# Optimization experiments

Hardware: AMD Instinct MI355X
Metric: run time of the kernel (lower is better)

Reference implementation:

```python
import jax, jax.numpy as jnp
import numpy as np

T, D, DFF, E, K = 2048, 1024, 2816, 8, 2


def setup_inputs() -> dict:
    key = jax.random.key(0)
    k1, k2, k3, k4, k5, k6 = jax.random.split(key, 6)
    return {
        "x": jax.random.normal(k1, (T, D), dtype=jnp.float32),
        "topk_weight": jax.random.uniform(k2, (T, K), dtype=jnp.float32),
        "gate_w": jax.random.normal(k3, (E, DFF, D), dtype=jnp.float32) * 0.02,
        "up_w": jax.random.normal(k4, (E, DFF, D), dtype=jnp.float32) * 0.02,
        "down_w": jax.random.normal(k5, (E, D, DFF), dtype=jnp.float32) * 0.02,
        "topk_ids": jax.random.randint(k6, (T, K), 0, E, dtype=jnp.int64),
    }


def reference(x, topk_weight, gate_w, up_w, down_w, topk_ids):
    # x: [T, D]; topk_ids/topk_weight: [T, K]
    # Per expert: SwiGLU MLP over all tokens, combined with the per-token
    # routing weight for that expert (0 if the expert was not selected).
    out = jnp.zeros_like(x)
    num_experts = gate_w.shape[0]
    for e in range(num_experts):
        h = jax.nn.silu(x @ gate_w[e].T) * (x @ up_w[e].T)  # [T, DFF]
        y = h @ down_w[e].T                                  # [T, D]
        # sum over top-k slots of routing weight where this expert was chosen
        w_e = jnp.sum(jnp.where(topk_ids == e, topk_weight, 0.0), axis=1)  # [T]
        out = out + y * w_e[:, None]
    return out
```

## Files before the change

kernel.cpp:

```cpp
#include <hip/hip_runtime.h>
#include <stdint.h>

typedef __attribute__((ext_vector_type(8))) __bf16 bf16x8;
typedef __attribute__((ext_vector_type(4))) float f32x4;
typedef __attribute__((ext_vector_type(8))) unsigned short ushort8;

#define T_TOK 2048
#define D_DIM 1024
#define DFF   2816
#define NEXP  8
#define NROWS 4096
#define BK    32
#define NW_ELEM (NEXP * DFF * D_DIM)
#define MAXTM2 24

#define SWZ(r,g) ((g) ^ (((r) >> 1) & 3))

#define TL_N    0
#define TL_BASE 16
#define TL_VAL  80
#define TL_EXP  144

__device__ __forceinline__ void lds_cp16(const void* g, void* l) {
  __builtin_amdgcn_global_load_lds(
      (const __attribute__((address_space(1))) void*)g,
      (__attribute__((address_space(3))) void*)l, 16, 0, 0);
}

__device__ __forceinline__ ushort8 pack_bf16x8(float4 a, float4 b) {
  union { __bf16 h[8]; ushort8 u; } r;
  r.h[0] = (__bf16)a.x; r.h[1] = (__bf16)a.y; r.h[2] = (__bf16)a.z; r.h[3] = (__bf16)a.w;
  r.h[4] = (__bf16)b.x; r.h[5] = (__bf16)b.y; r.h[6] = (__bf16)b.z; r.h[7] = (__bf16)b.w;
  return r.u;
}

__device__ __forceinline__ unsigned short f2bf(float f) {
  union { __bf16 h; unsigned short u; } r;
  r.h = (__bf16)f;
  return r.u;
}

__global__ __launch_bounds__(512) void routing_kernel(
    const int* __restrict__ ids, const float* __restrict__ w,
    int* __restrict__ cnt, int* __restrict__ off,
    int* __restrict__ tok, float* __restrict__ wgt, int* __restrict__ rowmap,
    int* __restrict__ tl2)
{
  __shared__ int s_cnt[NEXP];
  __shared__ int s_off[NEXP];
  const int lane = threadIdx.x & 63;
  const int e    = threadIdx.x >> 6;

  int total = 0;
  for (int c = 0; c < NROWS / 64; ++c) {
    int id = ids[c * 64 + lane];
    unsigned long long b = __ballot(id == e);
    total += __popcll(b);
  }
  if (lane == 0) s_cnt[e] = total;
  __syncthreads();
  if (threadIdx.x == 0) {
    int acc = 0, n2 = 0;
    for (int i = 0; i < NEXP; ++i) {
      s_off[i] = acc; off[i] = acc; cnt[i] = s_cnt[i];
      for (int j = 0; j < s_cnt[i]; j += 256) {
        tl2[TL_BASE + n2] = acc + j;
        tl2[TL_VAL  + n2] = min(256, s_cnt[i] - j);
        tl2[TL_EXP  + n2] = i;
        ++n2;
      }
      acc += s_cnt[i];
    }
    tl2[TL_N] = n2;
  }
  __syncthreads();
  int base = s_off[e];
  for (int c = 0; c < NROWS / 64; ++c) {
    int idx = c * 64 + lane;
    int id = ids[idx];
    bool m = (id == e);
    unsigned long long b = __ballot(m);
    int pos = __popcll(b & ((1ull << lane) - 1ull));
    if (m) {
      tok[base + pos] = idx >> 1;
      wgt[base + pos] = w[idx];
      rowmap[idx] = base + pos;
    }
    base += __popcll(b);
  }
}

__global__ __launch_bounds__(256) void gather_x_kernel(
    const float* __restrict__ x, const int* __restrict__ tok,
    unsigned short* __restrict__ xg)
{
  const int i = blockIdx.x;
  const int t = tok[i];
  const float4 v = ((const float4*)(x + (size_t)t * D_DIM))[threadIdx.x];
  ushort4 o;
  o.x = f2bf(v.x); o.y = f2bf(v.y); o.z = f2bf(v.z); o.w = f2bf(v.w);
  ((ushort4*)(xg + (size_t)i * D_DIM))[threadIdx.x] = o;
}

__global__ __launch_bounds__(256) void wconv_gu_kernel(
    const float* __restrict__ gw, const float* __restrict__ uw,
    unsigned short* __restrict__ gb, unsigned short* __restrict__ ub)
{
  const size_t n = NW_ELEM / 8;
  const size_t stride = (size_t)gridDim.x * blockDim.x;
  for (size_t i = (size_t)blockIdx.x * blockDim.x + threadIdx.x;
       i < 2 * n; i += stride) {
    const bool up = (i >= n);
    const size_t idx = (up ? i - n : i) * 8;
    const float* src = up ? uw : gw;
    unsigned short* dst = up ? ub : gb;
    float4 a = *(const float4*)(src + idx);
    float4 b = *(const float4*)(src + idx + 4);
    *(ushort8*)(dst + idx) = pack_bf16x8(a, b);
  }
}

#define BM_A 256
#define BN_A 64
#define NT_A (DFF / BN_A)
#define NWORK_A (MAXTM2 * NT_A)
#define WCD_BLKS 1024
#define NWG_A (NWORK_A + WCD_BLKS)
#define KT_A (D_DIM / BK)

__global__ __launch_bounds__(512) void moe_gateup_bf(
    const unsigned short* __restrict__ gbuf, const unsigned short* __restrict__ ubuf,
    const unsigned short* __restrict__ xg, const float* __restrict__ wgt,
    const int* __restrict__ tl2,
    unsigned short* __restrict__ hbuf,
    const float* __restrict__ down_w, unsigned short* __restrict__ dbuf)
{
  const int bid = blockIdx.x;
  const int ntm = tl2[TL_N];
  const int nwork = ntm * NT_A;
  const int tid = threadIdx.x;
  if (bid >= nwork) {
    if (bid >= NWORK_A) {
      const int c = bid - NWORK_A;
      const size_t stride = (size_t)WCD_BLKS * 512;
      for (size_t i = (size_t)c * 512 + tid; i < NW_ELEM / 8; i += stride) {
        const size_t idx = i * 8;
        float4 a = *(const float4*)(down_w + idx);
        float4 b = *(const float4*)(down_w + idx + 4);
        *(ushort8*)(dbuf + idx) = pack_bf16x8(a, b);
      }
    }
    return;
  }
  const int tile = bid % ntm;
  const int nt   = bid / ntm;
  const int row_base = tl2[TL_BASE + tile];
  const int valid    = tl2[TL_VAL  + tile];
  const int e        = tl2[TL_EXP  + tile];
  const int n0 = nt * BN_A;

  __shared__ __align__(16) unsigned short Alds[2][BM_A * BK];
  __shared__ __align__(16) unsigned short Bg[2][BN_A * BK];
  __shared__ __align__(16) unsigned short Bu[2][BN_A * BK];

  const int lane = tid & 63;
  const int wid = tid >> 6;
  const int wm = wid >> 1, wn = wid & 1;
  const int lhi = lane >> 4, llo = lane & 15;

  f32x4 accg[4][2], accu[4][2];
  #pragma unroll
  for (int i = 0; i < 4; ++i)
    #pragma unroll
    for (int j = 0; j < 2; ++j) {
      accg[i][j] = (f32x4){0.f, 0.f, 0.f, 0.f};
      accu[i][j] = (f32x4){0.f, 0.f, 0.f, 0.f};
    }

  const unsigned short* gb = gbuf + ((size_t)e * DFF + n0) * D_DIM;
  const unsigned short* ub = ubuf + ((size_t)e * DFF + n0) * D_DIM;

  const int ar0 = tid >> 2, ag = tid & 3;
  const int ar1 = ar0 + 128;
  const size_t a_src0 = (size_t)(row_base + min(ar0, valid - 1)) * D_DIM + SWZ(ar0, ag) * 8;
  const size_t a_src1 = (size_t)(row_base + min(ar1, valid - 1)) * D_DIM + SWZ(ar1, ag) * 8;
  const int q = tid & 255;
  const int br = q >> 2, bg2 = q & 3;
  const size_t b_src = (size_t)br * D_DIM + SWZ(br, bg2) * 8;
  const unsigned short* bsrc_base = (tid < 256) ? gb : ub;
  unsigned short* bdst0 = (tid < 256) ? &Bg[0][q * 8] : &Bu[0][q * 8];
  unsigned short* bdst1 = (tid < 256) ? &Bg[1][q * 8] : &Bu[1][q * 8];

  lds_cp16(xg + a_src0, &Alds[0][tid * 8]);
  lds_cp16(xg + a_src1, &Alds[0][(tid + 512) * 8]);
  lds_cp16(bsrc_base + b_src, bdst0);
  __syncthreads();

  for (int t = 0; t < KT_A; ++t) {
    const int cur = t & 1;
    const int kn = (t + 1 < KT_A) ? (t + 1) * BK : 0;

    lds_cp16(xg + a_src0 + kn, &Alds[cur ^ 1][tid * 8]);
    lds_cp16(xg + a_src1 + kn, &Alds[cur ^ 1][(tid + 512) * 8]);
    lds_cp16(bsrc_base + b_src + kn, cur ? bdst0 : bdst1);

    bf16x8 a[4], bgf[2], buf_[2];
    #pragma unroll
    for (int mi = 0; mi < 4; ++mi) {
      int row = wm * 64 + mi * 16 + llo;
      a[mi] = *(const bf16x8*)&Alds[cur][row * BK + SWZ(row, lhi) * 8];
    }
    #pragma unroll
    for (int ni = 0; ni < 2; ++ni) {
      int row = wn * 32 + ni * 16 + llo;
      bgf[ni]  = *(const bf16x8*)&Bg[cur][row * BK + SWZ(row, lhi) * 8];
      buf_[ni] = *(const bf16x8*)&Bu[cur][row * BK + SWZ(row, lhi) * 8];
    }
    #pragma unroll
    for (int mi = 0; mi < 4; ++mi)
      #pragma unroll
      for (int ni = 0; ni < 2; ++ni) {
        accg[mi][ni] = __builtin_amdgcn_mfma_f32_16x16x32_bf16(a[mi], bgf[ni], accg[mi][ni], 0, 0, 0);
        accu[mi][ni] = __builtin_amdgcn_mfma_f32_16x16x32_bf16(a[mi], buf_[ni], accu[mi][ni], 0, 0, 0);
      }
    __syncthreads();
  }

  #pragma unroll
  for (int mi = 0; mi < 4; ++mi) {
    #pragma unroll
    for (int r = 0; r < 4; ++r) {
      int row = wm * 64 + mi * 16 + lhi * 4 + r;
      if (row < valid) {
        int grow = row_base + row;
        float wv = wgt[grow];
        size_t base = (size_t)grow * DFF + n0 + wn * 32;
        #pragma unroll
        for (int ni = 0; ni < 2; ++ni) {
          float g = accg[mi][ni][r];
          float u = accu[mi][ni][r];
          float h = (g / (1.f + __expf(-g))) * u * wv;
          hbuf[base + ni * 16 + llo] = f2bf(h);
        }
      }
    }
  }
}

#define BM_B 256
#define BN_B 128
#define NT_B (D_DIM / BN_B)
#define SLICES_B 4
#define NWG_B (MAXTM2 * NT_B * SLICES_B)

template <bool USE_YBUF>
__global__ __launch_bounds__(512) void moe_down_bf(
    const unsigned short* __restrict__ dbuf,
    const unsigned short* __restrict__ hbuf,
    const int* __restrict__ tok,
    const int* __restrict__ tl2,
    float* __restrict__ ybuf_or_out)
{
  constexpr int KS = DFF / SLICES_B;
  constexpr int KT = KS / BK;

  const int bid = blockIdx.x;
  const int ntm = tl2[TL_N];
  const int nwork = ntm * NT_B * SLICES_B;
  if (bid >= nwork) return;
  const int tile = bid % ntm;
  const int r1_  = bid / ntm;
  const int nt = r1_ % NT_B;
  const int sl = r1_ / NT_B;
  const int row_base = tl2[TL_BASE + tile];
  const int valid    = tl2[TL_VAL  + tile];
  const int e        = tl2[TL_EXP  + tile];
  const int n0 = nt * BN_B;
  const int kbeg = sl * KS;

  __shared__ __align__(16) unsigned short Alds[2][BM_B * BK];
  __shared__ __align__(16) unsigned short Blds[2][BN_B * BK];

  const int tid = threadIdx.x, lane = tid & 63, wid = tid >> 6;
  const int wm = wid >> 1, wn = wid & 1;
  const int lhi = lane >> 4, llo = lane & 15;

  f32x4 acc[4][4];
  #pragma unroll
  for (int i = 0; i < 4; ++i)
    #pragma unroll
    for (int j = 0; j < 4; ++j) acc[i][j] = (f32x4){0.f, 0.f, 0.f, 0.f};

  const unsigned short* db = dbuf + ((size_t)e * D_DIM + n0) * DFF;

  const int ar0 = tid >> 2, ag = tid & 3;
  const int ar1 = ar0 + 128;
  const size_t a_src0 = (size_t)(row_base + min(ar0, valid - 1)) * DFF + SWZ(ar0, ag) * 8;
  const size_t a_src1 = (size_t)(row_base + min(ar1, valid - 1)) * DFF + SWZ(ar1, ag) * 8;
  const int brr = tid >> 2, bgg = tid & 3;
  const size_t b_src = (size_t)brr * DFF + SWZ(brr, bgg) * 8;

  lds_cp16(hbuf + a_src0 + kbeg, &Alds[0][tid * 8]);
  lds_cp16(hbuf + a_src1 + kbeg, &Alds[0][(tid + 512) * 8]);
  lds_cp16(db + b_src + kbeg, &Blds[0][tid * 8]);
  __syncthreads();

  for (int t = 0; t < KT; ++t) {
    const int cur = t & 1, nxt = cur ^ 1;
    const int kn = kbeg + ((t + 1 < KT) ? (t + 1) * BK : 0);

    lds_cp16(hbuf + a_src0 + kn, &Alds[nxt][tid * 8]);
    lds_cp16(hbuf + a_src1 + kn, &Alds[nxt][(tid + 512) * 8]);
    lds_cp16(db + b_src + kn, &Blds[nxt][tid * 8]);

    bf16x8 a[4], b[4];
    #pragma unroll
    for (int mi = 0; mi < 4; ++mi) {
      int row = wm * 64 + mi * 16 + llo;
      a[mi] = *(const bf16x8*)&Alds[cur][row * BK + SWZ(row, lhi) * 8];
    }
    #pragma unroll
    for (int ni = 0; ni < 4; ++ni) {
      int row = wn * 64 + ni * 16 + llo;
      b[ni] = *(const bf16x8*)&Blds[cur][row * BK + SWZ(row, lhi) * 8];
    }
    #pragma unroll
    for (int mi = 0; mi < 4; ++mi)
      #pragma unroll
      for (int ni = 0; ni < 4; ++ni)
        acc[mi][ni] = __builtin_amdgcn_mfma_f32_16x16x32_bf16(a[mi], b[ni], acc[mi][ni], 0, 0, 0);
    __syncthreads();
  }

  #pragma unroll
  for (int mi = 0; mi < 4; ++mi) {
    #pragma unroll
    for (int r = 0; r < 4; ++r) {
      int row = wm * 64 + mi * 16 + lhi * 4 + r;
      if (row < valid) {
        if (USE_YBUF) {
          float* yp = ybuf_or_out + ((size_t)sl * NROWS + row_base + row) * D_DIM + n0 + wn * 64;
          #pragma unroll
          for (int ni = 0; ni < 4; ++ni) yp[ni * 16 + llo] = acc[mi][ni][r];
        } else {
          int tk = tok[row_base + row];
          float* op = ybuf_or_out + (size_t)tk * D_DIM + n0 + wn * 64;
          #pragma unroll
          for (int ni = 0; ni < 4; ++ni) atomicAdd(op + ni * 16 + llo, acc[mi][ni][r]);
        }
      }
    }
  }
}

__global__ __launch_bounds__(256) void combine_kernel(
    const float* __restrict__ ybuf, const int* __restrict__ rowmap,
    float* __restrict__ out)
{
  const int t = blockIdx.x;
  const int d = threadIdx.x * 4;
  const int r0 = rowmap[t * 2], r1 = rowmap[t * 2 + 1];
  float4 s = {0.f, 0.f, 0.f, 0.f};
  #pragma unroll
  for (int sl = 0; sl < SLICES_B; ++sl) {
    const float4 a = *(const float4*)(ybuf + ((size_t)sl * NROWS + r0) * D_DIM + d);
    const float4 b = *(const float4*)(ybuf + ((size_t)sl * NROWS + r1) * D_DIM + d);
    s.x += a.x + b.x; s.y += a.y + b.y; s.z += a.z + b.z; s.w += a.w + b.w;
  }
  *(float4*)(out + (size_t)t * D_DIM + d) = s;
}

extern "C" void kernel_launch(void* const* d_in, const int* in_sizes, int n_in,
                              void* d_out, int out_size, void* d_ws, size_t ws_size,
                              hipStream_t stream) {
  const float* x      = (const float*)d_in[0];
  const float* topk_w = (const float*)d_in[1];
  const float* gate_w = (const float*)d_in[2];
  const float* up_w   = (const float*)d_in[3];
  const float* down_w = (const float*)d_in[4];
  const int*   ids    = (const int*)d_in[5];
  float* out = (float*)d_out;

  char* ws = (char*)d_ws;
  int*   cnt    = (int*)(ws + 0);
  int*   off    = (int*)(ws + 32);
  int*   tok    = (int*)(ws + 64);
  float* wgt    = (float*)(ws + 64 + NROWS * 4);
  int*   rowmap = (int*)(ws + 64 + NROWS * 8);
  int*   tl2    = (int*)(ws + 50688);

  const size_t XG_OFF = 65536;
  const size_t XG_SZ  = (size_t)NROWS * D_DIM * 2;
  const size_t HB_OFF = XG_OFF + XG_SZ;
  const size_t HB_SZ  = (size_t)NROWS * DFF * 2;
  const size_t W_SZ   = (size_t)NW_ELEM * 2;
  const size_t GB_OFF = HB_OFF + HB_SZ;
  const size_t UB_OFF = GB_OFF + W_SZ;
  const size_t DB_OFF = UB_OFF + W_SZ;
  const size_t YB_OFF = DB_OFF + W_SZ;
  const size_t YB_SZ  = (size_t)SLICES_B * NROWS * D_DIM * 4;

  unsigned short* xg   = (unsigned short*)(ws + XG_OFF);
  unsigned short* hbuf = (unsigned short*)(ws + HB_OFF);
  unsigned short* gbuf = (unsigned short*)(ws + GB_OFF);
  unsigned short* ubuf = (unsigned short*)(ws + UB_OFF);
  unsigned short* dbuf = (unsigned short*)(ws + DB_OFF);
  float* ybuf = (float*)(ws + YB_OFF);

  routing_kernel<<<1, 512, 0, stream>>>(ids, topk_w, cnt, off, tok, wgt, rowmap, tl2);
  gather_x_kernel<<<NROWS, 256, 0, stream>>>(x, tok, xg);
  wconv_gu_kernel<<<4096, 256, 0, stream>>>(gate_w, up_w, gbuf, ubuf);
  moe_gateup_bf<<<NWG_A, 512, 0, stream>>>(gbuf, ubuf, xg, wgt, tl2, hbuf, down_w, dbuf);

  if (ws_size >= YB_OFF + YB_SZ) {
    moe_down_bf<true><<<NWG_B, 512, 0, stream>>>(dbuf, hbuf, tok, tl2, ybuf);
    combine_kernel<<<T_TOK, 256, 0, stream>>>(ybuf, rowmap, out);
  } else {
    hipMemsetAsync(d_out, 0, (size_t)out_size * sizeof(float), stream);
    moe_down_bf<false><<<NWG_B, 512, 0, stream>>>(dbuf, hbuf, tok, tl2, out);
  }
}
```

Before: 257.9 us.

## Triple-buffer LDS GEMM pipelines and store split-K partials as bf16

```diff
diff --git a/kernel.cpp b/kernel.cpp
--- a/kernel.cpp
+++ b/kernel.cpp
@@ -39,6 +39,16 @@
   r.h = (__bf16)f;
   return r.u;
 }
+
+__device__ __forceinline__ float bf2f(unsigned short u) {
+  union { uint32_t u; float f; } v; v.u = (uint32_t)u << 16;
+  return v.f;
+}
+
+#define PIPE_BARRIER_VM3() do { \
+    asm volatile("s_waitcnt vmcnt(3)" ::: "memory"); \
+    __builtin_amdgcn_s_barrier(); \
+  } while (0)
 
 __global__ __launch_bounds__(512) void routing_kernel(
     const int* __restrict__ ids, const float* __restrict__ w,
@@ -159,9 +169,9 @@
   const int e        = tl2[TL_EXP  + tile];
   const int n0 = nt * BN_A;
 
-  __shared__ __align__(16) unsigned short Alds[2][BM_A * BK];
-  __shared__ __align__(16) unsigned short Bg[2][BN_A * BK];
-  __shared__ __align__(16) unsigned short Bu[2][BN_A * BK];
+  __shared__ __align__(16) unsigned short Alds[3][BM_A * BK];
+  __shared__ __align__(16) unsigned short Bg[3][BN_A * BK];
+  __shared__ __align__(16) unsigned short Bu[3][BN_A * BK];
 
   const int lane = tid & 63;
   const int wid = tid >> 6;
@@ -188,21 +198,30 @@
   const int br = q >> 2, bg2 = q & 3;
   const size_t b_src = (size_t)br * D_DIM + SWZ(br, bg2) * 8;
   const unsigned short* bsrc_base = (tid < 256) ? gb : ub;
-  unsigned short* bdst0 = (tid < 256) ? &Bg[0][q * 8] : &Bu[0][q * 8];
-  unsigned short* bdst1 = (tid < 256) ? &Bg[1][q * 8] : &Bu[1][q * 8];
+  unsigned short* bdst[3];
+  bdst[0] = (tid < 256) ? &Bg[0][q * 8] : &Bu[0][q * 8];
+  bdst[1] = (tid < 256) ? &Bg[1][q * 8] : &Bu[1][q * 8];
+  bdst[2] = (tid < 256) ? &Bg[2][q * 8] : &Bu[2][q * 8];
 
   lds_cp16(xg + a_src0, &Alds[0][tid * 8]);
   lds_cp16(xg + a_src1, &Alds[0][(tid + 512) * 8]);
-  lds_cp16(bsrc_base + b_src, bdst0);
-  __syncthreads();
-
+  lds_cp16(bsrc_base + b_src, bdst[0]);
+  {
+    const int k1 = BK;
+    lds_cp16(xg + a_src0 + k1, &Alds[1][tid * 8]);
+    lds_cp16(xg + a_src1 + k1, &Alds[1][(tid + 512) * 8]);
+    lds_cp16(bsrc_base + b_src + k1, bdst[1]);
+  }
+
+  int cur = 0;
   for (int t = 0; t < KT_A; ++t) {
-    const int cur = t & 1;
-    const int kn = (t + 1 < KT_A) ? (t + 1) * BK : 0;
-
-    lds_cp16(xg + a_src0 + kn, &Alds[cur ^ 1][tid * 8]);
-    lds_cp16(xg + a_src1 + kn, &Alds[cur ^ 1][(tid + 512) * 8]);
-    lds_cp16(bsrc_base + b_src + kn, cur ? bdst0 : bdst1);
+    PIPE_BARRIER_VM3();
+
+    const int nb = (cur + 2 >= 3) ? cur - 1 : cur + 2;
+    const int kn = (t + 2 < KT_A) ? (t + 2) * BK : 0;
+    lds_cp16(xg + a_src0 + kn, &Alds[nb][tid * 8]);
+    lds_cp16(xg + a_src1 + kn, &Alds[nb][(tid + 512) * 8]);
+    lds_cp16(bsrc_base + b_src + kn, bdst[nb]);
 
     bf16x8 a[4], bgf[2], buf_[2];
     #pragma unroll
@@ -223,7 +242,8 @@
         accg[mi][ni] = __builtin_amdgcn_mfma_f32_16x16x32_bf16(a[mi], bgf[ni], accg[mi][ni], 0, 0, 0);
         accu[mi][ni] = __builtin_amdgcn_mfma_f32_16x16x32_bf16(a[mi], buf_[ni], accu[mi][ni], 0, 0, 0);
       }
-    __syncthreads();
+
+    cur = (cur + 1 >= 3) ? 0 : cur + 1;
   }
 
   #pragma unroll
@@ -259,7 +279,7 @@
     const unsigned short* __restrict__ hbuf,
     const int* __restrict__ tok,
     const int* __restrict__ tl2,
-    float* __restrict__ ybuf_or_out)
+    unsigned short* __restrict__ ybuf, float* __restrict__ out_atomic)
 {
   constexpr int KS = DFF / SLICES_B;
   constexpr int KT = KS / BK;
@@ -278,8 +298,8 @@
   const int n0 = nt * BN_B;
   const int kbeg = sl * KS;
 
-  __shared__ __align__(16) unsigned short Alds[2][BM_B * BK];
-  __shared__ __align__(16) unsigned short Blds[2][BN_B * BK];
+  __shared__ __align__(16) unsigned short Alds[3][BM_B * BK];
+  __shared__ __align__(16) unsigned short Blds[3][BN_B * BK];
 
   const int tid = threadIdx.x, lane = tid & 63, wid = tid >> 6;
   const int wm = wid >> 1, wn = wid & 1;
@@ -303,15 +323,22 @@
   lds_cp16(hbuf + a_src0 + kbeg, &Alds[0][tid * 8]);
   lds_cp16(hbuf + a_src1 + kbeg, &Alds[0][(tid + 512) * 8]);
   lds_cp16(db + b_src + kbeg, &Blds[0][tid * 8]);
-  __syncthreads();
-
+  {
+    const int k1 = kbeg + BK;
+    lds_cp16(hbuf + a_src0 + k1, &Alds[1][tid * 8]);
+    lds_cp16(hbuf + a_src1 + k1, &Alds[1][(tid + 512) * 8]);
+    lds_cp16(db + b_src + k1, &Blds[1][tid * 8]);
+  }
+
+  int cur = 0;
   for (int t = 0; t < KT; ++t) {
-    const int cur = t & 1, nxt = cur ^ 1;
-    const int kn = kbeg + ((t + 1 < KT) ? (t + 1) * BK : 0);
-
-    lds_cp16(hbuf + a_src0 + kn, &Alds[nxt][tid * 8]);
-    lds_cp16(hbuf + a_src1 + kn, &Alds[nxt][(tid + 512) * 8]);
-    lds_cp16(db + b_src + kn, &Blds[nxt][tid * 8]);
+    PIPE_BARRIER_VM3();
+
+    const int nb = (cur + 2 >= 3) ? cur - 1 : cur + 2;
+    const int kn = kbeg + ((t + 2 < KT) ? (t + 2) * BK : 0);
+    lds_cp16(hbuf + a_src0 + kn, &Alds[nb][tid * 8]);
+    lds_cp16(hbuf + a_src1 + kn, &Alds[nb][(tid + 512) * 8]);
+    lds_cp16(db + b_src + kn, &Blds[nb][tid * 8]);
 
     bf16x8 a[4], b[4];
     #pragma unroll
@@ -329,7 +356,8 @@
       #pragma unroll
       for (int ni = 0; ni < 4; ++ni)
         acc[mi][ni] = __builtin_amdgcn_mfma_f32_16x16x32_bf16(a[mi], b[ni], acc[mi][ni], 0, 0, 0);
-    __syncthreads();
+
+    cur = (cur + 1 >= 3) ? 0 : cur + 1;
   }
 
   #pragma unroll
@@ -339,12 +367,12 @@
       int row = wm * 64 + mi * 16 + lhi * 4 + r;
       if (row < valid) {
         if (USE_YBUF) {
-          float* yp = ybuf_or_out + ((size_t)sl * NROWS + row_base + row) * D_DIM + n0 + wn * 64;
+          unsigned short* yp = ybuf + ((size_t)sl * NROWS + row_base + row) * D_DIM + n0 + wn * 64;
           #pragma unroll
-          for (int ni = 0; ni < 4; ++ni) yp[ni * 16 + llo] = acc[mi][ni][r];
+          for (int ni = 0; ni < 4; ++ni) yp[ni * 16 + llo] = f2bf(acc[mi][ni][r]);
         } else {
           int tk = tok[row_base + row];
-          float* op = ybuf_or_out + (size_t)tk * D_DIM + n0 + wn * 64;
+          float* op = out_atomic + (size_t)tk * D_DIM + n0 + wn * 64;
           #pragma unroll
           for (int ni = 0; ni < 4; ++ni) atomicAdd(op + ni * 16 + llo, acc[mi][ni][r]);
         }
@@ -354,19 +382,23 @@
 }
 
 __global__ __launch_bounds__(256) void combine_kernel(
-    const float* __restrict__ ybuf, const int* __restrict__ rowmap,
+    const unsigned short* __restrict__ ybuf, const int* __restrict__ rowmap,
     float* __restrict__ out)
 {
   const int t = blockIdx.x;
   const int d = threadIdx.x * 4;
   const int r0 = rowmap[t * 2], r1 = rowmap[t * 2 + 1];
-  float4 s = {0.f, 0.f, 0.f, 0.f};
+  float s0 = 0.f, s1 = 0.f, s2 = 0.f, s3 = 0.f;
   #pragma unroll
   for (int sl = 0; sl < SLICES_B; ++sl) {
-    const float4 a = *(const float4*)(ybuf + ((size_t)sl * NROWS + r0) * D_DIM + d);
-    const float4 b = *(const float4*)(ybuf + ((size_t)sl * NROWS + r1) * D_DIM + d);
-    s.x += a.x + b.x; s.y += a.y + b.y; s.z += a.z + b.z; s.w += a.w + b.w;
-  }
+    ushort4 a = *(const ushort4*)(ybuf + ((size_t)sl * NROWS + r0) * D_DIM + d);
+    ushort4 b = *(const ushort4*)(ybuf + ((size_t)sl * NROWS + r1) * D_DIM + d);
+    s0 += bf2f(a.x) + bf2f(b.x);
+    s1 += bf2f(a.y) + bf2f(b.y);
+    s2 += bf2f(a.z) + bf2f(b.z);
+    s3 += bf2f(a.w) + bf2f(b.w);
+  }
+  float4 s = {s0, s1, s2, s3};
   *(float4*)(out + (size_t)t * D_DIM + d) = s;
 }
 
@@ -398,14 +430,14 @@
   const size_t UB_OFF = GB_OFF + W_SZ;
   const size_t DB_OFF = UB_OFF + W_SZ;
   const size_t YB_OFF = DB_OFF + W_SZ;
-  const size_t YB_SZ  = (size_t)SLICES_B * NROWS * D_DIM * 4;
+  const size_t YB_SZ  = (size_t)SLICES_B * NROWS * D_DIM * 2;
 
   unsigned short* xg   = (unsigned short*)(ws + XG_OFF);
   unsigned short* hbuf = (unsigned short*)(ws + HB_OFF);
   unsigned short* gbuf = (unsigned short*)(ws + GB_OFF);
   unsigned short* ubuf = (unsigned short*)(ws + UB_OFF);
   unsigned short* dbuf = (unsigned short*)(ws + DB_OFF);
-  float* ybuf = (float*)(ws + YB_OFF);
+  unsigned short* ybuf = (unsigned short*)(ws + YB_OFF);
 
   routing_kernel<<<1, 512, 0, stream>>>(ids, topk_w, cnt, off, tok, wgt, rowmap, tl2);
   gather_x_kernel<<<NROWS, 256, 0, stream>>>(x, tok, xg);
@@ -413,10 +445,10 @@
   moe_gateup_bf<<<NWG_A, 512, 0, stream>>>(gbuf, ubuf, xg, wgt, tl2, hbuf, down_w, dbuf);
 
   if (ws_size >= YB_OFF + YB_SZ) {
-    moe_down_bf<true><<<NWG_B, 512, 0, stream>>>(dbuf, hbuf, tok, tl2, ybuf);
+    moe_down_bf<true><<<NWG_B, 512, 0, stream>>>(dbuf, hbuf, tok, tl2, ybuf, nullptr);
     combine_kernel<<<T_TOK, 256, 0, stream>>>(ybuf, rowmap, out);
   } else {
     hipMemsetAsync(d_out, 0, (size_t)out_size * sizeof(float), stream);
-    moe_down_bf<false><<<NWG_B, 512, 0, stream>>>(dbuf, hbuf, tok, tl2, out);
-  }
-}
+    moe_down_bf<false><<<NWG_B, 512, 0, stream>>>(dbuf, hbuf, tok, tl2, nullptr, out);
+  }
+}
```

Result: faster. 242.3 us (-6.1%).
